# Kernel tuning notes

Measured on AMD Instinct MI355X. Metric: run time of the kernel, lower is better.

The kernel has to match this reference:

```python
import jax, jax.numpy as jnp
import numpy as np

N_NODES = 50000
N_EDGES = 800000
D_IN = 96
HID = 128


def _glorot(key, shape):
    fan_in, fan_out = shape[0], shape[1]
    lim = np.sqrt(6.0 / (fan_in + fan_out)).astype(np.float32)
    return jax.random.uniform(key, shape, jnp.float32, -lim, lim)


def setup_inputs() -> dict:
    key = jax.random.key(0)
    ks = jax.random.split(key, 12)
    x = jax.random.normal(ks[0], (N_NODES, D_IN), jnp.float32)
    edge_index = jax.random.randint(ks[1], (2, N_EDGES), 0, N_NODES)
    return {
        "x": x,
        "edge_index": edge_index,
        "W_in": _glorot(ks[2], (D_IN, HID)),
        "b_in": jnp.zeros((HID,), jnp.float32),
        "W1": _glorot(ks[3], (HID, HID)),
        "b1": jnp.zeros((HID,), jnp.float32),
        "W2": _glorot(ks[4], (HID, HID)),
        "b2": jnp.zeros((HID,), jnp.float32),
        "Wm1": _glorot(ks[5], (2 * HID, HID)),
        "bm1": jnp.zeros((HID,), jnp.float32),
        "Wm2": _glorot(ks[6], (HID, 1)),
        "bm2": jnp.zeros((1,), jnp.float32),
    }


def _gcn_conv(h, W, b, src, dst, n_nodes):
    # PyG GCNConv with add_self_loops=True, normalize=True:
    # out = D^{-1/2} (A + I) D^{-1/2} (h W) + b, aggregating x_j (source) into dst.
    loop = jnp.arange(n_nodes)
    row = jnp.concatenate([src, loop])  # source / j
    col = jnp.concatenate([dst, loop])  # target / i
    deg = jax.ops.segment_sum(jnp.ones(row.shape, h.dtype), col, num_segments=n_nodes)
    dinv = jnp.where(deg > 0, jax.lax.rsqrt(deg), 0.0)
    norm = dinv[row] * dinv[col]  # [E+N]
    xw = h @ W  # [N, H]
    msg = xw[row] * norm[:, None]  # gather + scale, [E+N, H]
    out = jax.ops.segment_sum(msg, col, num_segments=n_nodes)  # scatter-add
    return out + b


def reference(x, edge_index, W_in, b_in, W1, b1, W2, b2, Wm1, bm1, Wm2, bm2):
    src, dst = edge_index[0], edge_index[1]
    n = x.shape[0]
    h = jax.nn.relu(x @ W_in + b_in)  # dropout is identity at inference
    h = jax.nn.relu(_gcn_conv(h, W1, b1, src, dst, n))
    h = jax.nn.relu(_gcn_conv(h, W2, b2, src, dst, n))
    ef = jnp.concatenate([h[src], h[dst]], axis=1)  # [E, 2H]
    hid = jax.nn.relu(ef @ Wm1 + bm1)
    logits = (hid @ Wm2 + bm2)[:, 0]  # [E]
    return logits
```

## Files before the change

kernel.cpp:

```cpp
#include <hip/hip_runtime.h>

#define N_NODES 50000
#define N_EDGES 800000
#define D_IN 96
#define HID 128
#define NB 391
#define BCAP 3072
#define AECAP 1408

typedef __attribute__((ext_vector_type(8))) _Float16 halfx8;
typedef __attribute__((ext_vector_type(4))) _Float16 half4v;
typedef __attribute__((ext_vector_type(2))) _Float16 half2v;
typedef __attribute__((ext_vector_type(16))) float f32x16;

__device__ inline float dot2acc(half2v a, half2v b, float c) {
#if __has_builtin(__builtin_amdgcn_fdot2)
    return __builtin_amdgcn_fdot2(a, b, c, false);
#else
    return c + (float)a[0] * (float)b[0] + (float)a[1] * (float)b[1];
#endif
}

__device__ inline halfx8 relu8(halfx8 s) {
#if __has_builtin(__builtin_elementwise_max)
    return __builtin_elementwise_max(s, (halfx8)0);
#else
    halfx8 r;
#pragma unroll
    for (int i = 0; i < 8; i++) r[i] = s[i] > (_Float16)0 ? s[i] : (_Float16)0;
    return r;
#endif
}

__global__ __launch_bounds__(256) void hist_pack_kernel(const int* __restrict__ dst,
                                                        int* __restrict__ bhist,
                                                        const float* __restrict__ W_in,
                                                        const float* __restrict__ W1,
                                                        const float* __restrict__ W2,
                                                        const float* __restrict__ Wm1,
                                                        const float* __restrict__ Wm2,
                                                        _Float16* __restrict__ packed) {
    __shared__ int lh[NB];
    int t = threadIdx.x;
    if (blockIdx.x < 196) {
        for (int i = t; i < NB; i += 256) lh[i] = 0;
        __syncthreads();
        int base = blockIdx.x * 4096;
#pragma unroll
        for (int i = 0; i < 16; i++) {
            int e = base + i * 256 + t;
            if (e < N_EDGES) atomicAdd(&lh[dst[e] >> 7], 1);
        }
        __syncthreads();
        for (int i = t; i < NB; i += 256) atomicAdd(&bhist[i], lh[i]);
        return;
    }
    int g = (blockIdx.x - 196) * 256 + t;
    if (g >= 77952) return;
    if (g >= 77824) { packed[g] = (_Float16)Wm2[g - 77824]; return; }
    const float* Wsrc;
    int K, u;
    if (g < 12288)      { Wsrc = W_in;            K = 96;  u = g; }
    else if (g < 28672) { Wsrc = W1;              K = 128; u = g - 12288; }
    else if (g < 45056) { Wsrc = W2;              K = 128; u = g - 28672; }
    else if (g < 61440) { Wsrc = Wm1;             K = 128; u = g - 45056; }
    else                { Wsrc = Wm1 + 128 * 128; K = 128; u = g - 61440; }
    int steps = K >> 4;
    int cb = u / (steps * 512);
    int rem = u - cb * steps * 512;
    int s = rem >> 9;
    int lane = (rem >> 3) & 63;
    int j = rem & 7;
    int k = s * 16 + ((lane >> 5) << 3) + j;
    int n = (cb << 5) + (lane & 31);
    packed[g] = (_Float16)Wsrc[k * 128 + n];
}

__global__ __launch_bounds__(512) void scan_buckets_kernel(const int* __restrict__ bhist,
                                                           int* __restrict__ boff,
                                                           int* __restrict__ bcursor) {
    __shared__ int s[512];
    int t = threadIdx.x;
    int v = (t < NB) ? bhist[t] : 0;
    s[t] = v;
    __syncthreads();
    for (int off = 1; off < 512; off <<= 1) {
        int u = (t >= off) ? s[t - off] : 0;
        __syncthreads();
        s[t] += u;
        __syncthreads();
    }
    if (t < NB) {
        int ex = s[t] - v;
        boff[t] = ex;
        bcursor[t] = ex;
    }
    if (t == NB - 1) boff[NB] = s[t];
}

__global__ __launch_bounds__(512) void bin_kernel(const int* __restrict__ src,
                                                  const int* __restrict__ dst,
                                                  int* __restrict__ bcursor,
                                                  unsigned long long* __restrict__ binned) {
    __shared__ int lh[NB];
    __shared__ int gbs[NB];
    int t = threadIdx.x;
    for (int i = t; i < NB; i += 512) lh[i] = 0;
    __syncthreads();
    int base = blockIdx.x * 8192;
    unsigned long long pk[16];
    int bb[16], rk[16];
#pragma unroll
    for (int i = 0; i < 16; i++) {
        int e = base + i * 512 + t;
        bb[i] = -1;
        if (e < N_EDGES) {
            int s = src[e], d = dst[e];
            int b = d >> 7;
            bb[i] = b;
            pk[i] = ((unsigned long long)s << 27) |
                    ((unsigned long long)(d & 127) << 20) | (unsigned long long)e;
            rk[i] = atomicAdd(&lh[b], 1);
        }
    }
    __syncthreads();
    for (int i = t; i < NB; i += 512) gbs[i] = atomicAdd(&bcursor[i], lh[i]);
    __syncthreads();
#pragma unroll
    for (int i = 0; i < 16; i++) {
        if (bb[i] >= 0) binned[gbs[bb[i]] + rk[i]] = pk[i];
    }
}

__global__ __launch_bounds__(256) void bucket_sort_kernel(const unsigned long long* __restrict__ binned,
                                                          const int* __restrict__ boff,
                                                          int* __restrict__ ce_src,
                                                          int* __restrict__ ce_eid,
                                                          int* __restrict__ ce_dst,
                                                          int* __restrict__ csr_ptr,
                                                          float* __restrict__ dinv) {
    __shared__ int2 sorted[BCAP];
    __shared__ int cntA[128], sc[128];
    int b = blockIdx.x;
    int t = threadIdx.x;
    int base = boff[b];
    int k = boff[b + 1] - base;
    if (k > BCAP) k = BCAP;
    if (t < 128) cntA[t] = 0;
    __syncthreads();
    unsigned long long pk[12];
    int rk[12];
#pragma unroll
    for (int m = 0; m < 12; m++) {
        int i = t + m * 256;
        rk[m] = -1;
        if (i < k) {
            unsigned long long p = binned[base + i];
            pk[m] = p;
            int d = (int)((p >> 20) & 127);
            rk[m] = atomicAdd(&cntA[d], 1);
        }
    }
    __syncthreads();
    if (t < 128) sc[t] = cntA[t];
    __syncthreads();
    for (int off = 1; off < 128; off <<= 1) {
        int u = 0;
        if (t < 128 && t >= off) u = sc[t - off];
        __syncthreads();
        if (t < 128) sc[t] += u;
        __syncthreads();
    }
#pragma unroll
    for (int m = 0; m < 12; m++) {
        if (rk[m] >= 0) {
            unsigned long long p = pk[m];
            int d = (int)((p >> 20) & 127);
            int pos = sc[d] - cntA[d] + rk[m];
            int srcn = (int)(p >> 27);
            int eid = (int)(p & 0xFFFFF);
            sorted[pos] = make_int2(srcn | (d << 16), eid);
        }
    }
    __syncthreads();
    for (int i = t; i < k; i += 256) {
        int2 se = sorted[i];
        ce_src[base + i] = se.x & 0xFFFF;
        ce_eid[base + i] = se.y;
        ce_dst[base + i] = (b << 7) + (se.x >> 16);
    }
    if (t < 128) {
        int node = (b << 7) + t;
        if (node < N_NODES) {
            csr_ptr[node] = base + sc[t] - cntA[t];
            dinv[node] = 1.0f / sqrtf((float)(cntA[t] + 1));
        }
    }
    if (b == NB - 1 && t == 0) csr_ptr[N_NODES] = boff[NB];
}

__global__ __launch_bounds__(256) void fused_in_kernel(const float* __restrict__ x,
                                                       const _Float16* __restrict__ WpIn,
                                                       const _Float16* __restrict__ Wp1,
                                                       const float* __restrict__ b_in,
                                                       const float* __restrict__ dinv,
                                                       _Float16* __restrict__ y1, int M) {
    __shared__ _Float16 As[32 * 104];
    __shared__ _Float16 Hs[32 * 136];
    int tid = threadIdx.x;
    int M0 = blockIdx.x * 32;
    for (int i = tid; i < 32 * 24; i += 256) {
        int r = i / 24, c = i - r * 24;
        float4 v = make_float4(0.f, 0.f, 0.f, 0.f);
        int row = M0 + r;
        if (row < M) v = *(const float4*)&x[(size_t)row * 96 + c * 4];
        half2v a = {(_Float16)v.x, (_Float16)v.y};
        half2v b = {(_Float16)v.z, (_Float16)v.w};
        *(half2v*)&As[r * 104 + c * 4] = a;
        *(half2v*)&As[r * 104 + c * 4 + 2] = b;
    }
    __syncthreads();

    int wave = tid >> 6, lane = tid & 63;
    int col = wave * 32 + (lane & 31);
    {
        const halfx8* bp = (const halfx8*)WpIn + (size_t)wave * 6 * 64 + lane;
        const _Float16* arow = &As[(lane & 31) * 104 + ((lane >> 5) << 3)];
        f32x16 acc = {};
#pragma unroll
        for (int s = 0; s < 6; s++) {
            halfx8 a = *(const halfx8*)&arow[s * 16];
            acc = __builtin_amdgcn_mfma_f32_32x32x16_f16(a, bp[s * 64], acc, 0, 0, 0);
        }
        float bA = b_in[col];
#pragma unroll
        for (int r = 0; r < 16; r++) {
            int rl = (r & 3) + 8 * (r >> 2) + 4 * (lane >> 5);
            Hs[rl * 136 + col] = (_Float16)fmaxf(acc[r] + bA, 0.f);
        }
    }
    __syncthreads();
    {
        const halfx8* bp = (const halfx8*)Wp1 + (size_t)wave * 8 * 64 + lane;
        const _Float16* arow = &Hs[(lane & 31) * 136 + ((lane >> 5) << 3)];
        f32x16 acc = {};
#pragma unroll
        for (int s = 0; s < 8; s++) {
            halfx8 a = *(const halfx8*)&arow[s * 16];
            acc = __builtin_amdgcn_mfma_f32_32x32x16_f16(a, bp[s * 64], acc, 0, 0, 0);
        }
#pragma unroll
        for (int r = 0; r < 16; r++) {
            int rl = (r & 3) + 8 * (r >> 2) + 4 * (lane >> 5);
            int grow = M0 + rl;
            if (grow < M) {
                y1[((size_t)wave * N_NODES + grow) * 32 + (lane & 31)] =
                    (_Float16)(acc[r] * dinv[grow]);
            }
        }
    }
}

__global__ __launch_bounds__(256) void gemm_f16_kernel(const _Float16* __restrict__ A,
                                                       const _Float16* __restrict__ Wp,
                                                       const float* __restrict__ bias,
                                                       const float* __restrict__ rowscale,
                                                       _Float16* __restrict__ out,
                                                       int M, int steps, int dorelu) {
    const int K = 128;
    __shared__ _Float16 As[32 * 136];
    int tid = threadIdx.x;
    int M0 = blockIdx.x * 32;
    int stride = K + 8;
    for (int i = tid; i < 32 * 16; i += 256) {
        int r = i >> 4, c = i & 15;
        uint4 v = make_uint4(0, 0, 0, 0);
        int row = M0 + r;
        if (row < M)
            v = *(const uint4*)&A[((size_t)(c >> 2) * N_NODES + row) * 32 + (c & 3) * 8];
        *(uint4*)&As[r * stride + c * 8] = v;
    }
    __syncthreads();

    int wave = tid >> 6, lane = tid & 63;
    const halfx8* bp = (const halfx8*)Wp + (size_t)wave * steps * 64 + lane;
    const _Float16* arow = &As[(lane & 31) * stride + ((lane >> 5) << 3)];
    f32x16 acc = {};
    for (int s = 0; s < steps; s++) {
        halfx8 a = *(const halfx8*)&arow[s * 16];
        acc = __builtin_amdgcn_mfma_f32_32x32x16_f16(a, bp[s * 64], acc, 0, 0, 0);
    }
    int col = wave * 32 + (lane & 31);
    float bA = bias ? bias[col] : 0.f;
#pragma unroll
    for (int r = 0; r < 16; r++) {
        int rl = (r & 3) + 8 * (r >> 2) + 4 * (lane >> 5);
        int grow = M0 + rl;
        if (grow < M) {
            float sc = rowscale ? rowscale[grow] : 1.f;
            float v0 = (acc[r] + bA) * sc;
            if (dorelu) v0 = fmaxf(v0, 0.f);
            out[((size_t)wave * N_NODES + grow) * 32 + (lane & 31)] = (_Float16)v0;
        }
    }
}

__global__ __launch_bounds__(256) void gemm_uv_kernel(const _Float16* __restrict__ A,
                                                      const _Float16* __restrict__ WpU,
                                                      const _Float16* __restrict__ WpV,
                                                      const float* __restrict__ bm1,
                                                      _Float16* __restrict__ U,
                                                      _Float16* __restrict__ V,
                                                      int M) {
    const int K = 128, steps = 8;
    __shared__ _Float16 As[32 * 136];
    int tid = threadIdx.x;
    int M0 = blockIdx.x * 32;
    int stride = K + 8;
    for (int i = tid; i < 32 * 16; i += 256) {
        int r = i >> 4, c = i & 15;
        uint4 v = make_uint4(0, 0, 0, 0);
        int row = M0 + r;
        if (row < M)
            v = *(const uint4*)&A[((size_t)(c >> 2) * N_NODES + row) * 32 + (c & 3) * 8];
        *(uint4*)&As[r * stride + c * 8] = v;
    }
    __syncthreads();

    int wave = tid >> 6, lane = tid & 63;
    const halfx8* bu = (const halfx8*)WpU + (size_t)wave * steps * 64 + lane;
    const halfx8* bv = (const halfx8*)WpV + (size_t)wave * steps * 64 + lane;
    const _Float16* arow = &As[(lane & 31) * stride + ((lane >> 5) << 3)];
    f32x16 au = {}, av = {};
#pragma unroll
    for (int s = 0; s < steps; s++) {
        halfx8 a = *(const halfx8*)&arow[s * 16];
        au = __builtin_amdgcn_mfma_f32_32x32x16_f16(a, bu[s * 64], au, 0, 0, 0);
        av = __builtin_amdgcn_mfma_f32_32x32x16_f16(a, bv[s * 64], av, 0, 0, 0);
    }
    int col = wave * 32 + (lane & 31);
    float bA = bm1[col];
#pragma unroll
    for (int r = 0; r < 16; r++) {
        int rl = (r & 3) + 8 * (r >> 2) + 4 * (lane >> 5);
        int grow = M0 + rl;
        if (grow < M) {
            U[(size_t)grow * 128 + col] = (_Float16)(au[r] + bA);
            V[(size_t)grow * 128 + col] = (_Float16)av[r];
        }
    }
}

__global__ __launch_bounds__(256, 6) void aggregate_kernel(const _Float16* __restrict__ y,
                                                           const float* __restrict__ dinv,
                                                           const int* __restrict__ ptr,
                                                           const int* __restrict__ ce_src,
                                                           const float* __restrict__ bias,
                                                           _Float16* __restrict__ out) {
    __shared__ int sidx[AECAP];
    __shared__ int sptr[65];
    int b = blockIdx.x;
    int sl = (b & 7) >> 1;
    int o = ((b >> 3) << 1) + (b & 1);
    int node0 = o * 64;
    int tid = threadIdx.x;
    if (tid < 65) {
        int nn = node0 + tid;
        sptr[tid] = ptr[nn < N_NODES ? nn : N_NODES];
    }
    __syncthreads();
    int base = sptr[0];
    int tot = sptr[64] - base;
    bool fit = (tot <= AECAP);
    if (fit) {
        for (int i = tid; i < tot; i += 256) sidx[i] = ce_src[base + i] << 6;
    }
    __syncthreads();

    int g = tid >> 2;
    int l = tid & 3;
    int nodeIdx = node0 + g;
    int node = nodeIdx < N_NODES ? nodeIdx : N_NODES - 1;
    float di = dinv[node];
    const char* ysl = (const char*)y + (size_t)sl * (N_NODES * 64) + (size_t)l * 16;
    halfx8 self = *(const halfx8*)(ysl + (size_t)node * 64);
    float a0 = (float)self[0], a1 = (float)self[1], a2 = (float)self[2], a3 = (float)self[3];
    float a4 = (float)self[4], a5 = (float)self[5], a6 = (float)self[6], a7 = (float)self[7];
    int s0 = sptr[g], s1 = sptr[g + 1];

    if (fit) {
        int j = s0 - base, e = s1 - base;
        for (; j + 7 < e; j += 8) {
            halfx8 v0 = *(const halfx8*)(ysl + sidx[j]);
            halfx8 v1 = *(const halfx8*)(ysl + sidx[j + 1]);
            halfx8 v2 = *(const halfx8*)(ysl + sidx[j + 2]);
            halfx8 v3 = *(const halfx8*)(ysl + sidx[j + 3]);
            halfx8 v4 = *(const halfx8*)(ysl + sidx[j + 4]);
            halfx8 v5 = *(const halfx8*)(ysl + sidx[j + 5]);
            halfx8 v6 = *(const halfx8*)(ysl + sidx[j + 6]);
            halfx8 v7 = *(const halfx8*)(ysl + sidx[j + 7]);
            __builtin_amdgcn_sched_barrier(0);
            a0 += (float)v0[0] + (float)v1[0] + (float)v2[0] + (float)v3[0]
                + (float)v4[0] + (float)v5[0] + (float)v6[0] + (float)v7[0];
            a1 += (float)v0[1] + (float)v1[1] + (float)v2[1] + (float)v3[1]
                + (float)v4[1] + (float)v5[1] + (float)v6[1] + (float)v7[1];
            a2 += (float)v0[2] + (float)v1[2] + (float)v2[2] + (float)v3[2]
                + (float)v4[2] + (float)v5[2] + (float)v6[2] + (float)v7[2];
            a3 += (float)v0[3] + (float)v1[3] + (float)v2[3] + (float)v3[3]
                + (float)v4[3] + (float)v5[3] + (float)v6[3] + (float)v7[3];
            a4 += (float)v0[4] + (float)v1[4] + (float)v2[4] + (float)v3[4]
                + (float)v4[4] + (float)v5[4] + (float)v6[4] + (float)v7[4];
            a5 += (float)v0[5] + (float)v1[5] + (float)v2[5] + (float)v3[5]
                + (float)v4[5] + (float)v5[5] + (float)v6[5] + (float)v7[5];
            a6 += (float)v0[6] + (float)v1[6] + (float)v2[6] + (float)v3[6]
                + (float)v4[6] + (float)v5[6] + (float)v6[6] + (float)v7[6];
            a7 += (float)v0[7] + (float)v1[7] + (float)v2[7] + (float)v3[7]
                + (float)v4[7] + (float)v5[7] + (float)v6[7] + (float)v7[7];
        }
        for (; j + 3 < e; j += 4) {
            halfx8 v0 = *(const halfx8*)(ysl + sidx[j]);
            halfx8 v1 = *(const halfx8*)(ysl + sidx[j + 1]);
            halfx8 v2 = *(const halfx8*)(ysl + sidx[j + 2]);
            halfx8 v3 = *(const halfx8*)(ysl + sidx[j + 3]);
            __builtin_amdgcn_sched_barrier(0);
            a0 += (float)v0[0] + (float)v1[0] + (float)v2[0] + (float)v3[0];
            a1 += (float)v0[1] + (float)v1[1] + (float)v2[1] + (float)v3[1];
            a2 += (float)v0[2] + (float)v1[2] + (float)v2[2] + (float)v3[2];
            a3 += (float)v0[3] + (float)v1[3] + (float)v2[3] + (float)v3[3];
            a4 += (float)v0[4] + (float)v1[4] + (float)v2[4] + (float)v3[4];
            a5 += (float)v0[5] + (float)v1[5] + (float)v2[5] + (float)v3[5];
            a6 += (float)v0[6] + (float)v1[6] + (float)v2[6] + (float)v3[6];
            a7 += (float)v0[7] + (float)v1[7] + (float)v2[7] + (float)v3[7];
        }
        for (; j < e; j++) {
            halfx8 v = *(const halfx8*)(ysl + sidx[j]);
            a0 += (float)v[0]; a1 += (float)v[1]; a2 += (float)v[2]; a3 += (float)v[3];
            a4 += (float)v[4]; a5 += (float)v[5]; a6 += (float)v[6]; a7 += (float)v[7];
        }
    } else {
        for (int j = s0; j < s1; j++) {
            halfx8 v = *(const halfx8*)(ysl + ((size_t)ce_src[j] << 6));
            a0 += (float)v[0]; a1 += (float)v[1]; a2 += (float)v[2]; a3 += (float)v[3];
            a4 += (float)v[4]; a5 += (float)v[5]; a6 += (float)v[6]; a7 += (float)v[7];
        }
    }
    if (nodeIdx < N_NODES) {
        const float* bp = &bias[sl * 32 + l * 8];
        float4 bv0 = *(const float4*)bp;
        float4 bv1 = *(const float4*)(bp + 4);
        halfx8 ov;
        ov[0] = (_Float16)fmaxf(di * a0 + bv0.x, 0.f);
        ov[1] = (_Float16)fmaxf(di * a1 + bv0.y, 0.f);
        ov[2] = (_Float16)fmaxf(di * a2 + bv0.z, 0.f);
        ov[3] = (_Float16)fmaxf(di * a3 + bv0.w, 0.f);
        ov[4] = (_Float16)fmaxf(di * a4 + bv1.x, 0.f);
        ov[5] = (_Float16)fmaxf(di * a5 + bv1.y, 0.f);
        ov[6] = (_Float16)fmaxf(di * a6 + bv1.z, 0.f);
        ov[7] = (_Float16)fmaxf(di * a7 + bv1.w, 0.f);
        *(halfx8*)&out[((size_t)sl * N_NODES + nodeIdx) * 32 + l * 8] = ov;
    }
}

__global__ __launch_bounds__(256) void edge_mlp_kernel(const _Float16* __restrict__ Ub,
                                                       const _Float16* __restrict__ Vb,
                                                       const int* __restrict__ ce_src,
                                                       const int* __restrict__ ce_eid,
                                                       const int* __restrict__ ce_dst,
                                                       const _Float16* __restrict__ Wm2h,
                                                       const float* __restrict__ bm2,
                                                       float* __restrict__ out) {
    __shared__ int ssrc[128], sdst[128], seid[128];
    int tid = threadIdx.x;
    int e0 = blockIdx.x * 128;
    if (tid < 128) {
        ssrc[tid] = ce_src[e0 + tid];
        seid[tid] = ce_eid[e0 + tid];
    } else {
        sdst[tid - 128] = ce_dst[e0 + tid - 128];
    }
    __syncthreads();
    int g = tid >> 4;
    int l = tid & 15;
    halfx8 wv = *(const halfx8*)&Wm2h[l * 8];
    half2v w0 = {wv[0], wv[1]}, w1 = {wv[2], wv[3]}, w2 = {wv[4], wv[5]}, w3 = {wv[6], wv[7]};
    halfx8 uu[8], vv[8];
#pragma unroll
    for (int k = 0; k < 8; k++) {
        int e = g + 16 * k;
        uu[k] = *(const halfx8*)&Ub[(size_t)ssrc[e] * 128 + l * 8];
        vv[k] = *(const halfx8*)&Vb[(size_t)sdst[e] * 128 + l * 8];
    }
    __builtin_amdgcn_sched_barrier(0);
    float p[8];
#pragma unroll
    for (int k = 0; k < 8; k++) {
        halfx8 s = relu8(uu[k] + vv[k]);
        half2v s0 = {s[0], s[1]}, s1 = {s[2], s[3]}, s2 = {s[4], s[5]}, s3 = {s[6], s[7]};
        float acc = dot2acc(s0, w0, 0.f);
        acc = dot2acc(s1, w1, acc);
        acc = dot2acc(s2, w2, acc);
        p[k] = dot2acc(s3, w3, acc);
    }
#pragma unroll
    for (int d = 1; d < 16; d <<= 1) {
#pragma unroll
        for (int k = 0; k < 8; k++) p[k] += __shfl_xor(p[k], d);
    }
    if (l == 0) {
        float bb = bm2[0];
#pragma unroll
        for (int k = 0; k < 8; k++) out[seid[g + 16 * k]] = p[k] + bb;
    }
}

extern "C" void kernel_launch(void* const* d_in, const int* in_sizes, int n_in,
                              void* d_out, int out_size, void* d_ws, size_t ws_size,
                              hipStream_t stream) {
    const float* x    = (const float*)d_in[0];
    const int* eidx   = (const int*)d_in[1];
    const float* W_in = (const float*)d_in[2];
    const float* b_in = (const float*)d_in[3];
    const float* W1   = (const float*)d_in[4];
    const float* b1   = (const float*)d_in[5];
    const float* W2   = (const float*)d_in[6];
    const float* b2   = (const float*)d_in[7];
    const float* Wm1  = (const float*)d_in[8];
    const float* bm1  = (const float*)d_in[9];
    const float* Wm2  = (const float*)d_in[10];
    const float* bm2  = (const float*)d_in[11];
    float* out = (float*)d_out;
    const int* src = eidx;
    const int* dst = eidx + N_EDGES;

    char* w = (char*)d_ws;
    size_t off = 0;
    auto alloc = [&](size_t bytes) -> char* {
        char* p = w + off;
        off = (off + bytes + 255) & ~(size_t)255;
        return p;
    };
    int* bhist    = (int*)alloc((size_t)NB * 4);
    int* boff     = (int*)alloc((size_t)(NB + 1) * 4);
    int* bcursor  = (int*)alloc((size_t)NB * 4);
    int* csr_ptr  = (int*)alloc((size_t)(N_NODES + 1) * 4);
    float* dinv   = (float*)alloc((size_t)N_NODES * 4);
    unsigned long long* binned = (unsigned long long*)alloc((size_t)N_EDGES * 8);
    int* ce_src   = (int*)alloc((size_t)N_EDGES * 4);
    int* ce_eid   = (int*)alloc((size_t)N_EDGES * 4);
    int* ce_dst   = (int*)alloc((size_t)N_EDGES * 4);
    _Float16* Wp  = (_Float16*)alloc((size_t)77952 * 2);
    _Float16* y1  = (_Float16*)alloc((size_t)N_NODES * HID * 2);
    _Float16* y2  = (_Float16*)alloc((size_t)N_NODES * HID * 2);
    _Float16* hbuf = (_Float16*)alloc((size_t)N_NODES * HID * 2);
    _Float16* Ub  = (_Float16*)alloc((size_t)N_NODES * HID * 2);
    _Float16* Vb  = (_Float16*)alloc((size_t)N_NODES * HID * 2);

    const _Float16* WpIn  = Wp;
    const _Float16* Wp1   = Wp + 12288;
    const _Float16* Wp2   = Wp + 28672;
    const _Float16* WpM1a = Wp + 45056;
    const _Float16* WpM1b = Wp + 61440;
    const _Float16* Wm2h  = Wp + 77824;

    hipMemsetAsync(bhist, 0, (size_t)NB * 4, stream);
    hist_pack_kernel<<<196 + 305, 256, 0, stream>>>(dst, bhist, W_in, W1, W2, Wm1, Wm2, Wp);
    scan_buckets_kernel<<<1, 512, 0, stream>>>(bhist, boff, bcursor);
    bin_kernel<<<98, 512, 0, stream>>>(src, dst, bcursor, binned);
    bucket_sort_kernel<<<NB, 256, 0, stream>>>(binned, boff, ce_src, ce_eid, ce_dst,
                                               csr_ptr, dinv);

    int gblocks = (N_NODES + 31) / 32;
    int ablocks = 782 * 4;
    fused_in_kernel<<<gblocks, 256, 0, stream>>>(x, WpIn, Wp1, b_in, dinv, y1, N_NODES);
    aggregate_kernel<<<ablocks, 256, 0, stream>>>(y1, dinv, csr_ptr, ce_src, b1, hbuf);
    gemm_f16_kernel<<<gblocks, 256, 0, stream>>>(hbuf, Wp2, nullptr, dinv, y2,
                                                 N_NODES, 8, 0);
    aggregate_kernel<<<ablocks, 256, 0, stream>>>(y2, dinv, csr_ptr, ce_src, b2, hbuf);
    gemm_uv_kernel<<<gblocks, 256, 0, stream>>>(hbuf, WpM1a, WpM1b, bm1, Ub, Vb, N_NODES);
    edge_mlp_kernel<<<N_EDGES / 128, 256, 0, stream>>>(Ub, Vb, ce_src, ce_eid, ce_dst,
                                                       Wm2h, bm2, out);
}
```

Baseline: 238.3 us.

## Slice U/V into 32-column panels and split edge MLP into partial-sum plus reduce

The U and V node tables are stored as four 32-column slices, mirroring the aggregate kernel's layout. The edge MLP is split into a per-slice partial kernel, whose blocks are interleaved so neighbouring blocks share a slice, and a small reduce kernel that sums the four partials, adds the bias and scatters to the original edge order. Each partial kernel's gathers touch a 4x smaller working set, aiming for better L2/MALL hit rates on the random src/dst gathers. The cost is an extra launch and a 12.8 MB round trip through the partial-sum buffer.

```diff
diff --git a/kernel.cpp b/kernel.cpp
--- a/kernel.cpp
+++ b/kernel.cpp
@@ -345,8 +345,8 @@
         int rl = (r & 3) + 8 * (r >> 2) + 4 * (lane >> 5);
         int grow = M0 + rl;
         if (grow < M) {
-            U[(size_t)grow * 128 + col] = (_Float16)(au[r] + bA);
-            V[(size_t)grow * 128 + col] = (_Float16)av[r];
+            U[((size_t)wave * N_NODES + grow) * 32 + (lane & 31)] = (_Float16)(au[r] + bA);
+            V[((size_t)wave * N_NODES + grow) * 32 + (lane & 31)] = (_Float16)av[r];
         }
     }
 }
@@ -461,55 +461,72 @@
     }
 }
 
-__global__ __launch_bounds__(256) void edge_mlp_kernel(const _Float16* __restrict__ Ub,
-                                                       const _Float16* __restrict__ Vb,
-                                                       const int* __restrict__ ce_src,
-                                                       const int* __restrict__ ce_eid,
-                                                       const int* __restrict__ ce_dst,
-                                                       const _Float16* __restrict__ Wm2h,
-                                                       const float* __restrict__ bm2,
-                                                       float* __restrict__ out) {
-    __shared__ int ssrc[128], sdst[128], seid[128];
+__global__ __launch_bounds__(256) void edge_part_kernel(const _Float16* __restrict__ U,
+                                                        const _Float16* __restrict__ V,
+                                                        const int* __restrict__ ce_src,
+                                                        const int* __restrict__ ce_dst,
+                                                        const _Float16* __restrict__ Wm2h,
+                                                        float* __restrict__ P) {
+    __shared__ int sS[128], sD[128];
+    int b = blockIdx.x;
+    int sl = (b & 7) >> 1;
+    int o = ((b >> 3) << 1) + (b & 1);
+    int e0 = o * 128;
     int tid = threadIdx.x;
-    int e0 = blockIdx.x * 128;
-    if (tid < 128) {
-        ssrc[tid] = ce_src[e0 + tid];
-        seid[tid] = ce_eid[e0 + tid];
-    } else {
-        sdst[tid - 128] = ce_dst[e0 + tid - 128];
-    }
-    __syncthreads();
-    int g = tid >> 4;
-    int l = tid & 15;
-    halfx8 wv = *(const halfx8*)&Wm2h[l * 8];
+    if (tid < 128) sS[tid] = ce_src[e0 + tid] << 6;
+    else sD[tid - 128] = ce_dst[e0 + tid - 128] << 6;
+    __syncthreads();
+    int g = tid >> 2;
+    int l = tid & 3;
+    const char* Ub = (const char*)U + (size_t)sl * (N_NODES * 64) + (size_t)l * 16;
+    const char* Vb = (const char*)V + (size_t)sl * (N_NODES * 64) + (size_t)l * 16;
+    halfx8 wv = *(const halfx8*)&Wm2h[sl * 32 + l * 8];
     half2v w0 = {wv[0], wv[1]}, w1 = {wv[2], wv[3]}, w2 = {wv[4], wv[5]}, w3 = {wv[6], wv[7]};
-    halfx8 uu[8], vv[8];
-#pragma unroll
-    for (int k = 0; k < 8; k++) {
-        int e = g + 16 * k;
-        uu[k] = *(const halfx8*)&Ub[(size_t)ssrc[e] * 128 + l * 8];
-        vv[k] = *(const halfx8*)&Vb[(size_t)sdst[e] * 128 + l * 8];
-    }
+
+    halfx8 u0 = *(const halfx8*)(Ub + sS[g]);
+    halfx8 v0 = *(const halfx8*)(Vb + sD[g]);
+    halfx8 u1 = *(const halfx8*)(Ub + sS[g + 64]);
+    halfx8 v1 = *(const halfx8*)(Vb + sD[g + 64]);
     __builtin_amdgcn_sched_barrier(0);
-    float p[8];
-#pragma unroll
-    for (int k = 0; k < 8; k++) {
-        halfx8 s = relu8(uu[k] + vv[k]);
+    float pp[2];
+    {
+        halfx8 s = relu8(u0 + v0);
         half2v s0 = {s[0], s[1]}, s1 = {s[2], s[3]}, s2 = {s[4], s[5]}, s3 = {s[6], s[7]};
         float acc = dot2acc(s0, w0, 0.f);
         acc = dot2acc(s1, w1, acc);
         acc = dot2acc(s2, w2, acc);
-        p[k] = dot2acc(s3, w3, acc);
-    }
-#pragma unroll
-    for (int d = 1; d < 16; d <<= 1) {
-#pragma unroll
-        for (int k = 0; k < 8; k++) p[k] += __shfl_xor(p[k], d);
-    }
-    if (l == 0) {
-        float bb = bm2[0];
-#pragma unroll
-        for (int k = 0; k < 8; k++) out[seid[g + 16 * k]] = p[k] + bb;
+        pp[0] = dot2acc(s3, w3, acc);
+    }
+    {
+        halfx8 s = relu8(u1 + v1);
+        half2v s0 = {s[0], s[1]}, s1 = {s[2], s[3]}, s2 = {s[4], s[5]}, s3 = {s[6], s[7]};
+        float acc = dot2acc(s0, w0, 0.f);
+        acc = dot2acc(s1, w1, acc);
+        acc = dot2acc(s2, w2, acc);
+        pp[1] = dot2acc(s3, w3, acc);
+    }
+#pragma unroll
+    for (int pass = 0; pass < 2; pass++) {
+        float p = pp[pass];
+        p += __shfl_xor(p, 1);
+        p += __shfl_xor(p, 2);
+        if (l == 0) P[(size_t)sl * N_EDGES + e0 + g + 64 * pass] = p;
+    }
+}
+
+__global__ __launch_bounds__(256) void edge_reduce_kernel(const float* __restrict__ P,
+                                                          const int* __restrict__ ce_eid,
+                                                          const float* __restrict__ bm2,
+                                                          float* __restrict__ out) {
+    float bb = bm2[0];
+    int i = blockIdx.x * 1024 + threadIdx.x;
+#pragma unroll
+    for (int k = 0; k < 4; k++, i += 256) {
+        if (i < N_EDGES) {
+            float p = P[i] + P[(size_t)N_EDGES + i] + P[(size_t)2 * N_EDGES + i]
+                    + P[(size_t)3 * N_EDGES + i] + bb;
+            out[ce_eid[i]] = p;
+        }
     }
 }
 
@@ -554,6 +571,7 @@
     _Float16* hbuf = (_Float16*)alloc((size_t)N_NODES * HID * 2);
     _Float16* Ub  = (_Float16*)alloc((size_t)N_NODES * HID * 2);
     _Float16* Vb  = (_Float16*)alloc((size_t)N_NODES * HID * 2);
+    float* Pbuf   = (float*)alloc((size_t)4 * N_EDGES * 4);
 
     const _Float16* WpIn  = Wp;
     const _Float16* Wp1   = Wp + 12288;
@@ -577,6 +595,6 @@
                                                  N_NODES, 8, 0);
     aggregate_kernel<<<ablocks, 256, 0, stream>>>(y2, dinv, csr_ptr, ce_src, b2, hbuf);
     gemm_uv_kernel<<<gblocks, 256, 0, stream>>>(hbuf, WpM1a, WpM1b, bm1, Ub, Vb, N_NODES);
-    edge_mlp_kernel<<<N_EDGES / 128, 256, 0, stream>>>(Ub, Vb, ce_src, ce_eid, ce_dst,
-                                                       Wm2h, bm2, out);
-}
+    edge_part_kernel<<<6250 * 4, 256, 0, stream>>>(Ub, Vb, ce_src, ce_dst, Wm2h, Pbuf);
+    edge_reduce_kernel<<<782, 256, 0, stream>>>(Pbuf, ce_eid, bm2, out);
+}
```

After: 244.3 us. 1.03x slower.
